# Performance work log

Measured on AMD Instinct MI355X. Metric: run time of the kernel, lower is better.

## Reference

```python
import jax, jax.numpy as jnp
import numpy as np

N = 50000   # nodes
F = 128     # v_feats
K = 128     # filters
H = 3       # multi_head
M = 10      # fixed neighbor count (hardcoded repeat(1,10,1) in source)


def setup_inputs() -> dict:
    key = jax.random.key(0)
    ks = jax.random.split(key, 10)
    vertices = jax.random.normal(ks[0], (N, F), jnp.float32)
    nh_indices = jax.random.randint(ks[1], (N, M), 0, N)
    int_indices = jax.random.randint(ks[2], (N, M), 0, N)
    nh_edges = jax.random.uniform(ks[3], (N, M), jnp.float32)
    int_edges = jax.random.uniform(ks[4], (N, M), jnp.float32)
    is_int = jax.random.randint(ks[5], (N,), 0, 2)
    scale = 0.05
    Wvc = jax.random.normal(ks[6], (H, F, K), jnp.float32) * scale
    Wvn_int = jax.random.normal(ks[7], (H, F, K), jnp.float32) * scale
    Wvn_nh = jax.random.normal(ks[8], (H, F, K), jnp.float32) * scale
    a = jax.random.normal(ks[9], (H, 2 * K, 1), jnp.float32) * scale
    bv = jnp.zeros((H, K), jnp.float32)
    return dict(vertices=vertices, nh_indices=nh_indices, int_indices=int_indices,
                nh_edges=nh_edges, int_edges=int_edges, is_int=is_int,
                Wvc=Wvc, bv=bv, Wvn_int=Wvn_int, Wvn_nh=Wvn_nh, a=a)


def reference(vertices, nh_indices, int_indices, nh_edges, int_edges, is_int,
              Wvc, bv, Wvn_int, Wvn_nh, a):
    n = vertices.shape[0]
    k = a.shape[1] // 2
    # Project center and neighbor features for all heads at once.
    Zc = jnp.einsum('nf,hfk->hnk', vertices, Wvc)        # [H,N,K]
    Vint = jnp.einsum('nf,hfk->hnk', vertices, Wvn_int)  # [H,N,K]
    Vnh = jnp.einsum('nf,hfk->hnk', vertices, Wvn_nh)    # [H,N,K]
    # cat((neighbor, center)) @ a  ==  neighbor @ a[:k] + center @ a[k:]
    a_n = a[:, :k, 0]  # [H,K]
    a_c = a[:, k:, 0]  # [H,K]
    e_center = jnp.einsum('hnk,hk->hn', Zc, a_c)[:, :, None]  # [H,N,1]

    def branch(Vside, idx, edges):
        mask = (idx != -1).astype(vertices.dtype)           # [N,M], -1 = pad
        g = Vside[:, idx]                                   # [H,N,M,K] gather
        e = jnp.einsum('hnmk,hk->hnm', g, a_n) + e_center   # [H,N,M]
        # faithful to source: scores zeroed (not -inf) by mask/edges before softmax
        e = e * mask[None] * edges[None]
        alpha = jax.nn.softmax(e, axis=2)                   # [H,N,M]
        norm = jnp.maximum(mask.sum(axis=1), 1.0)           # [N]
        Zn = jnp.einsum('hnmk,hnm->hnk', g * mask[None, :, :, None], alpha)
        return Zn / norm[None, :, None]

    Zn_inter = branch(Vint, int_indices, int_edges)
    Zn_chain = branch(Vnh, nh_indices, nh_edges)
    z = jax.nn.relu(Zc + Zn_inter + Zn_chain + bv[:, None, :])  # [H,N,K]
    # torch.cat(head outputs, dim=1) -> [N, H*K]
    return jnp.transpose(z, (1, 0, 2)).reshape(n, -1)
```

## Files before the change

### kernel.cpp

```cpp
#include <hip/hip_runtime.h>
#include <stdint.h>

#define N_V 50000
#define F_DIM 128
#define K_DIM 128
#define H_DIM 3
#define M_DIM 10
#define TILES_PER_BLK 4

using bf16x8 = __attribute__((ext_vector_type(8))) short;
using f32x4  = __attribute__((ext_vector_type(4))) float;
using f32x2  = __attribute__((ext_vector_type(2))) float;
using h4     = __attribute__((ext_vector_type(4))) _Float16;

__device__ inline unsigned short f2bf(float f) {
    union { float f; uint32_t u; } v; v.f = f;
    uint32_t u = v.u;
    u += 0x7fffu + ((u >> 16) & 1u);
    return (unsigned short)(u >> 16);
}

__device__ inline uint32_t pkh2(float a, float b) {
    union { _Float16 h[2]; uint32_t u; } v;
    v.h[0] = (_Float16)a; v.h[1] = (_Float16)b;
    return v.u;
}

#define LDS_AS __attribute__((address_space(3)))
__device__ inline void gl2lds16(const void* g, void* l) {
    __builtin_amdgcn_global_load_lds(
        (const __attribute__((address_space(1))) unsigned int*)g,
        (LDS_AS unsigned int*)l, 16, 0, 0);
}

#define WTOT (9 * 128 * 128)
#define XCH  (N_V * 16)
#define WACT (9 * 128)

__global__ void prep(const float* __restrict__ Wvc,
                     const float* __restrict__ Wvn_int,
                     const float* __restrict__ Wvn_nh,
                     const float* __restrict__ X,
                     const float* __restrict__ a,
                     unsigned short* __restrict__ Wt,
                     unsigned short* __restrict__ Xb,
                     unsigned short* __restrict__ wab) {
    int idx = blockIdx.x * 256 + threadIdx.x;
    if (idx < WTOT) {
        int b   = idx >> 14;
        int rem = idx & 16383;
        int k = rem >> 7;
        int f = rem & 127;
        int h = b / 3, t = b - 3 * h;
        const float* src = (t == 0) ? Wvc : (t == 1) ? Wvn_int : Wvn_nh;
        Wt[idx] = f2bf(src[(h * 128 + f) * 128 + k]);
        return;
    }
    int xi = idx - WTOT;
    if (xi < XCH) {
        const float4* Xv = (const float4*)X;
        float4 v0 = Xv[xi * 2];
        float4 v1 = Xv[xi * 2 + 1];
        uint4 o;
        o.x = (uint32_t)f2bf(v0.x) | ((uint32_t)f2bf(v0.y) << 16);
        o.y = (uint32_t)f2bf(v0.z) | ((uint32_t)f2bf(v0.w) << 16);
        o.z = (uint32_t)f2bf(v1.x) | ((uint32_t)f2bf(v1.y) << 16);
        o.w = (uint32_t)f2bf(v1.z) | ((uint32_t)f2bf(v1.w) << 16);
        *(uint4*)&Xb[(size_t)xi * 8] = o;
        return;
    }
    int wi = xi - XCH;
    if (wi < WACT) {
        int b = wi >> 7, f = wi & 127;
        int h = b / 3, t = b - 3 * h;
        const float* src = (t == 0) ? Wvc : (t == 1) ? Wvn_int : Wvn_nh;
        const float4* wrow = (const float4*)&src[(h * 128 + f) * 128];
        const float4* av   = (const float4*)&a[h * 256 + (t == 0 ? 128 : 0)];
        float acc = 0.f;
        #pragma unroll 8
        for (int c = 0; c < 32; ++c) {
            float4 w = wrow[c], x = av[c];
            acc += w.x * x.x + w.y * x.y + w.z * x.z + w.w * x.w;
        }
        wab[b * 128 + f] = f2bf(acc);
    }
}

__global__ __launch_bounds__(256, 3) void gemm_kernel(
    const unsigned short* __restrict__ Xb,
    const unsigned short* __restrict__ Wt,
    const unsigned short* __restrict__ wab,
    _Float16* __restrict__ zc16,
    uint8_t* __restrict__ Vint,
    uint8_t* __restrict__ Vnh,
    float* __restrict__ ec4,
    float* __restrict__ ei4,
    float* __restrict__ en4) {
    __shared__ unsigned short As[2][64 * 128];

    const int tid  = threadIdx.x;
    const int b    = blockIdx.y;
    const int hh   = b / 3;
    const int tt   = b - 3 * hh;
    const int wv   = tid >> 6;
    const int lane = tid & 63;
    const int q    = lane >> 4;
    const int ln   = lane & 15;
    const int cb   = (wv >> 1) * 64;
    const int rb   = (wv & 1) * 32;
    const int m0   = blockIdx.x * (64 * TILES_PER_BLK);

    auto stage = [&](int buf, int tile) {
        const int mb = m0 + tile * 64;
        #pragma unroll
        for (int it = 0; it < 4; ++it) {
            int c16 = it * 256 + tid;
            int r   = c16 >> 4;
            int p   = c16 & 15;
            int lch = p ^ (r & 15);
            int gr  = mb + r;
            if (gr >= N_V) gr = 0;
            gl2lds16(Xb + (size_t)gr * 128 + lch * 8, &As[buf][c16 * 8]);
        }
    };

    stage(0, 0);

    const unsigned short* Wb = Wt + (size_t)b * 16384;
    bf16x8 bfr[4][4];
    #pragma unroll
    for (int ct = 0; ct < 4; ++ct) {
        int col = cb + 4 * ln + ct;
        #pragma unroll
        for (int kk = 0; kk < 4; ++kk)
            bfr[ct][kk] = *(const bf16x8*)&Wb[col * 128 + kk * 32 + q * 8];
    }

    const bool do_e = (b == 0) && (wv < 2);
    bf16x8 wz[4];
    if (do_e) {
        #pragma unroll
        for (int kk = 0; kk < 4; ++kk) {
            bf16x8 z = {0, 0, 0, 0, 0, 0, 0, 0};
            if (ln < 9) z = *(const bf16x8*)&wab[ln * 128 + kk * 32 + q * 8];
            wz[kk] = z;
        }
    }

    __syncthreads();

    const int c0 = cb + 4 * ln;
    #pragma unroll
    for (int t = 0; t < TILES_PER_BLK; ++t) {
        const int mb = m0 + t * 64;

        if (t + 1 < TILES_PER_BLK) stage((t + 1) & 1, t + 1);

        bf16x8 afr[2][4];
        #pragma unroll
        for (int rt = 0; rt < 2; ++rt) {
            int r = rb + rt * 16 + ln;
            #pragma unroll
            for (int kk = 0; kk < 4; ++kk) {
                int p = (kk * 4 + q) ^ ln;
                afr[rt][kk] = *(const bf16x8*)&As[t & 1][r * 128 + p * 8];
            }
        }

        f32x4 acc[2][4];
        #pragma unroll
        for (int rt = 0; rt < 2; ++rt)
            #pragma unroll
            for (int ct = 0; ct < 4; ++ct) acc[rt][ct] = (f32x4){0.f, 0.f, 0.f, 0.f};

        #pragma unroll
        for (int rt = 0; rt < 2; ++rt)
            #pragma unroll
            for (int kk = 0; kk < 4; ++kk)
                #pragma unroll
                for (int ct = 0; ct < 4; ++ct)
                    acc[rt][ct] = __builtin_amdgcn_mfma_f32_16x16x32_bf16(
                        afr[rt][kk], bfr[ct][kk], acc[rt][ct], 0, 0, 0);

        if (do_e) {
            #pragma unroll
            for (int rt = 0; rt < 2; ++rt) {
                f32x4 ae = (f32x4){0.f, 0.f, 0.f, 0.f};
                #pragma unroll
                for (int kk = 0; kk < 4; ++kk)
                    ae = __builtin_amdgcn_mfma_f32_16x16x32_bf16(
                        afr[rt][kk], wz[kk], ae, 0, 0, 0);
                if (ln < 9) {
                    int h2 = ln / 3, t2 = ln - 3 * h2;
                    float* ep = (t2 == 0) ? ec4 : (t2 == 1) ? ei4 : en4;
                    #pragma unroll
                    for (int rg = 0; rg < 4; ++rg) {
                        int gr = mb + rb + rt * 16 + q * 4 + rg;
                        if (gr < N_V) ep[gr * 4 + h2] = ae[rg];
                    }
                }
            }
        }

        __syncthreads();

        if (tt == 0) {
            #pragma unroll
            for (int rt = 0; rt < 2; ++rt)
                #pragma unroll
                for (int rg = 0; rg < 4; ++rg) {
                    int gr = mb + rb + rt * 16 + q * 4 + rg;
                    if (gr >= N_V) continue;
                    uint2 s;
                    s.x = pkh2(acc[rt][0][rg], acc[rt][1][rg]);
                    s.y = pkh2(acc[rt][2][rg], acc[rt][3][rg]);
                    *(uint2*)&zc16[(size_t)gr * 384 + hh * 128 + c0] = s;
                }
        } else {
            uint8_t* Vside = (tt == 1) ? Vint : Vnh;
            #pragma unroll
            for (int rt = 0; rt < 2; ++rt)
                #pragma unroll
                for (int rg = 0; rg < 4; ++rg) {
                    int gr = mb + rb + rt * 16 + q * 4 + rg;
                    if (gr >= N_V) continue;
                    int pk = __builtin_amdgcn_cvt_pk_fp8_f32(
                        acc[rt][0][rg], acc[rt][1][rg], 0, false);
                    pk = __builtin_amdgcn_cvt_pk_fp8_f32(
                        acc[rt][2][rg], acc[rt][3][rg], pk, true);
                    *(uint32_t*)&Vside[((size_t)gr * 3 + hh) * 128 + c0] =
                        (uint32_t)pk;
                }
        }
    }
}

__global__ __launch_bounds__(256, 4) void attn_kernel(
    const int* __restrict__ nh_idx, const int* __restrict__ int_idx,
    const float* __restrict__ nh_edge, const float* __restrict__ int_edge,
    const float* __restrict__ bv,
    const uint8_t* __restrict__ Vint,
    const uint8_t* __restrict__ Vnh,
    const float* __restrict__ ec4, const float* __restrict__ ei4,
    const float* __restrict__ en4,
    const _Float16* __restrict__ zc16,
    float* __restrict__ out) {
    const int wv   = threadIdx.x >> 6;
    const int lane = threadIdx.x & 63;
    const int n    = blockIdx.x * 4 + wv;
    if (n >= N_V) return;
    const int g  = lane >> 4;
    const int gl = lane & 15;

    const bool part = (g <= 1) && (gl < M_DIM);
    int jm = -1; float wm = 0.f;
    if (part) {
        const int*   idx = (g == 0) ? int_idx  : nh_idx;
        const float* ed  = (g == 0) ? int_edge : nh_edge;
        jm = idx[n * M_DIM + gl];
        wm = ed[n * M_DIM + gl];
    }
    const bool  valid = part && (jm >= 0);
    const int   jc    = valid ? jm : 0;
    const float vfl   = valid ? 1.f : 0.f;

    const int src_base = (g < 2 ? 0 : 16) + (g & 1) * 5;
    int jrow[5];
    #pragma unroll
    for (int i = 0; i < 5; ++i) jrow[i] = __shfl(jc, src_base + i, 64);

    const uint8_t* Vb = (g < 2) ? Vint : Vnh;
    uint2 pv[3][5];
    #pragma unroll
    for (int i = 0; i < 5; ++i) {
        const uint8_t* base = Vb + (size_t)jrow[i] * 384 + gl * 8;
        #pragma unroll
        for (int h = 0; h < H_DIM; ++h)
            pv[h][i] = *(const uint2*)(base + h * 128);
    }
    float4 ev = make_float4(0.f, 0.f, 0.f, 0.f);
    if (part) ev = *(const float4*)&(((g == 0) ? ei4 : en4)[jc * 4]);
    const float4 ecv = *(const float4*)&ec4[n * 4];

    float4 zc[3], bb[3];
    if (g < 2) {
        #pragma unroll
        for (int h = 0; h < H_DIM; ++h) {
            h4 z = *(const h4*)&zc16[(size_t)n * 384 + h * 128 + gl * 8 + g * 4];
            zc[h] = make_float4((float)z[0], (float)z[1], (float)z[2], (float)z[3]);
            bb[h] = *(const float4*)&bv[h * 128 + gl * 8 + g * 4];
        }
    }

    float cf = vfl;
    #pragma unroll
    for (int off = 1; off < 16; off <<= 1) cf += __shfl_xor(cf, off, 64);
    const float cnorm = fmaxf(cf, 1.f);

    __builtin_amdgcn_sched_barrier(0);

    #pragma unroll
    for (int h = 0; h < H_DIM; ++h) {
        const float eh  = (h == 0) ? ev.x  : (h == 1) ? ev.y  : ev.z;
        const float ech = (h == 0) ? ecv.x : (h == 1) ? ecv.y : ecv.z;

        float l = (part && valid) ? (eh + ech) * wm : 0.f;
        float ex = part ? __expf(l) : 0.f;
        float sv = ex;
        #pragma unroll
        for (int off = 1; off < 16; off <<= 1) sv += __shfl_xor(sv, off, 64);
        float alphap = valid ? ex / (sv * cnorm) : 0.f;

        f32x2 acc2[4];
        #pragma unroll
        for (int c = 0; c < 4; ++c) acc2[c] = (f32x2){0.f, 0.f};
        #pragma unroll
        for (int i = 0; i < 5; ++i) {
            float al = __shfl(alphap, src_base + i, 64);
            f32x2 al2 = (f32x2){al, al};
            uint2 p  = pv[h][i];
            f32x2 f01 = __builtin_amdgcn_cvt_pk_f32_fp8(p.x, false);
            f32x2 f23 = __builtin_amdgcn_cvt_pk_f32_fp8(p.x, true);
            f32x2 f45 = __builtin_amdgcn_cvt_pk_f32_fp8(p.y, false);
            f32x2 f67 = __builtin_amdgcn_cvt_pk_f32_fp8(p.y, true);
            acc2[0] += al2 * f01;
            acc2[1] += al2 * f23;
            acc2[2] += al2 * f45;
            acc2[3] += al2 * f67;
        }
        #pragma unroll
        for (int c = 0; c < 4; ++c) {
            f32x2 v = acc2[c];
            v.x += __shfl_xor(v.x, 16, 64);
            v.y += __shfl_xor(v.y, 16, 64);
            v.x += __shfl_xor(v.x, 32, 64);
            v.y += __shfl_xor(v.y, 32, 64);
            acc2[c] = v;
        }
        if (g < 2) {
            size_t o = (size_t)n * 384 + h * 128 + gl * 8 + g * 4;
            float4 zn;
            if (g == 0) zn = make_float4(acc2[0].x, acc2[0].y, acc2[1].x, acc2[1].y);
            else        zn = make_float4(acc2[2].x, acc2[2].y, acc2[3].x, acc2[3].y);
            float4 r;
            r.x = fmaxf(zc[h].x + zn.x + bb[h].x, 0.f);
            r.y = fmaxf(zc[h].y + zn.y + bb[h].y, 0.f);
            r.z = fmaxf(zc[h].z + zn.z + bb[h].z, 0.f);
            r.w = fmaxf(zc[h].w + zn.w + bb[h].w, 0.f);
            *(float4*)&out[o] = r;
        }
    }
}

extern "C" void kernel_launch(void* const* d_in, const int* in_sizes, int n_in,
                              void* d_out, int out_size, void* d_ws, size_t ws_size,
                              hipStream_t stream) {
    const float* vertices    = (const float*)d_in[0];
    const int*   nh_indices  = (const int*)d_in[1];
    const int*   int_indices = (const int*)d_in[2];
    const float* nh_edges    = (const float*)d_in[3];
    const float* int_edges   = (const float*)d_in[4];
    const float* Wvc     = (const float*)d_in[6];
    const float* bv      = (const float*)d_in[7];
    const float* Wvn_int = (const float*)d_in[8];
    const float* Wvn_nh  = (const float*)d_in[9];
    const float* a       = (const float*)d_in[10];
    float* out = (float*)d_out;

    char* ws = (char*)d_ws;
    size_t off = 0;
    unsigned short* Wt = (unsigned short*)(ws + off);
    off += (size_t)WTOT * 2;                  off = (off + 255) & ~(size_t)255;
    unsigned short* wab = (unsigned short*)(ws + off);
    off += (size_t)WACT * 2;                  off = (off + 255) & ~(size_t)255;
    unsigned short* Xb = (unsigned short*)(ws + off);
    off += (size_t)N_V * 128 * 2;             off = (off + 255) & ~(size_t)255;
    uint8_t* Vint = (uint8_t*)(ws + off);
    off += (size_t)H_DIM * N_V * 128;         off = (off + 255) & ~(size_t)255;
    uint8_t* Vnh = (uint8_t*)(ws + off);
    off += (size_t)H_DIM * N_V * 128;         off = (off + 255) & ~(size_t)255;
    _Float16* zc16 = (_Float16*)(ws + off);
    off += (size_t)N_V * 384 * 2;             off = (off + 255) & ~(size_t)255;
    float* ec4 = (float*)(ws + off);
    off += (size_t)N_V * 4 * 4;               off = (off + 255) & ~(size_t)255;
    float* ei4 = (float*)(ws + off);
    off += (size_t)N_V * 4 * 4;               off = (off + 255) & ~(size_t)255;
    float* en4 = (float*)(ws + off);
    off += (size_t)N_V * 4 * 4;

    int prep_threads = WTOT + XCH + WACT;
    prep<<<(prep_threads + 255) / 256, 256, 0, stream>>>(
        Wvc, Wvn_int, Wvn_nh, vertices, a, Wt, Xb, wab);

    dim3 grid_g((N_V + 64 * TILES_PER_BLK - 1) / (64 * TILES_PER_BLK), 9);
    gemm_kernel<<<grid_g, 256, 0, stream>>>(Xb, Wt, wab, zc16, Vint, Vnh,
                                            ec4, ei4, en4);

    attn_kernel<<<(N_V + 3) / 4, 256, 0, stream>>>(
        nh_indices, int_indices, nh_edges, int_edges, bv,
        Vint, Vnh, ec4, ei4, en4, zc16, out);
}
```

Baseline: 230.7 us.

## Fuse bf16 conversion and attention-score projection into GEMM, drop prep kernel

Removes the separate prep kernel. The GEMM now reads fp32 vertices and weights directly and converts them to bf16 in registers before staging into LDS. The attention-score dot products are now computed from the GEMM accumulators times the coefficient vector, using shuffle reductions and LDS atomics, instead of a separate MFMA pass against precomputed W·a vectors. The grid is remapped to a 1D index with blocks grouped per XCD so that blocks sharing an X tile land on the same XCD for L2 reuse. The costs are synchronous global loads in place of async global-to-LDS copies, strided uncoalesced weight loads per block, and duplicated conversion work across the 9 head/type blocks.

Result: no change. 234.6 us (+1.7%).

```diff
diff --git a/kernel.cpp b/kernel.cpp
--- a/kernel.cpp
+++ b/kernel.cpp
@@ -1,4 +1,5 @@
 #include <hip/hip_runtime.h>
+#include <hip/hip_bf16.h>
 #include <stdint.h>
 
 #define N_V 50000
@@ -7,89 +8,33 @@
 #define H_DIM 3
 #define M_DIM 10
 #define TILES_PER_BLK 4
+#define NBLK 1764
+#define BLK_PER_XCD 221
+#define NBLK_PAD 1768
 
 using bf16x8 = __attribute__((ext_vector_type(8))) short;
 using f32x4  = __attribute__((ext_vector_type(4))) float;
 using f32x2  = __attribute__((ext_vector_type(2))) float;
 using h4     = __attribute__((ext_vector_type(4))) _Float16;
 
-__device__ inline unsigned short f2bf(float f) {
-    union { float f; uint32_t u; } v; v.f = f;
-    uint32_t u = v.u;
-    u += 0x7fffu + ((u >> 16) & 1u);
-    return (unsigned short)(u >> 16);
-}
-
 __device__ inline uint32_t pkh2(float a, float b) {
     union { _Float16 h[2]; uint32_t u; } v;
     v.h[0] = (_Float16)a; v.h[1] = (_Float16)b;
     return v.u;
 }
 
-#define LDS_AS __attribute__((address_space(3)))
-__device__ inline void gl2lds16(const void* g, void* l) {
-    __builtin_amdgcn_global_load_lds(
-        (const __attribute__((address_space(1))) unsigned int*)g,
-        (LDS_AS unsigned int*)l, 16, 0, 0);
-}
-
-#define WTOT (9 * 128 * 128)
-#define XCH  (N_V * 16)
-#define WACT (9 * 128)
-
-__global__ void prep(const float* __restrict__ Wvc,
-                     const float* __restrict__ Wvn_int,
-                     const float* __restrict__ Wvn_nh,
-                     const float* __restrict__ X,
-                     const float* __restrict__ a,
-                     unsigned short* __restrict__ Wt,
-                     unsigned short* __restrict__ Xb,
-                     unsigned short* __restrict__ wab) {
-    int idx = blockIdx.x * 256 + threadIdx.x;
-    if (idx < WTOT) {
-        int b   = idx >> 14;
-        int rem = idx & 16383;
-        int k = rem >> 7;
-        int f = rem & 127;
-        int h = b / 3, t = b - 3 * h;
-        const float* src = (t == 0) ? Wvc : (t == 1) ? Wvn_int : Wvn_nh;
-        Wt[idx] = f2bf(src[(h * 128 + f) * 128 + k]);
-        return;
-    }
-    int xi = idx - WTOT;
-    if (xi < XCH) {
-        const float4* Xv = (const float4*)X;
-        float4 v0 = Xv[xi * 2];
-        float4 v1 = Xv[xi * 2 + 1];
-        uint4 o;
-        o.x = (uint32_t)f2bf(v0.x) | ((uint32_t)f2bf(v0.y) << 16);
-        o.y = (uint32_t)f2bf(v0.z) | ((uint32_t)f2bf(v0.w) << 16);
-        o.z = (uint32_t)f2bf(v1.x) | ((uint32_t)f2bf(v1.y) << 16);
-        o.w = (uint32_t)f2bf(v1.z) | ((uint32_t)f2bf(v1.w) << 16);
-        *(uint4*)&Xb[(size_t)xi * 8] = o;
-        return;
-    }
-    int wi = xi - XCH;
-    if (wi < WACT) {
-        int b = wi >> 7, f = wi & 127;
-        int h = b / 3, t = b - 3 * h;
-        const float* src = (t == 0) ? Wvc : (t == 1) ? Wvn_int : Wvn_nh;
-        const float4* wrow = (const float4*)&src[(h * 128 + f) * 128];
-        const float4* av   = (const float4*)&a[h * 256 + (t == 0 ? 128 : 0)];
-        float acc = 0.f;
-        #pragma unroll 8
-        for (int c = 0; c < 32; ++c) {
-            float4 w = wrow[c], x = av[c];
-            acc += w.x * x.x + w.y * x.y + w.z * x.z + w.w * x.w;
-        }
-        wab[b * 128 + f] = f2bf(acc);
-    }
+__device__ inline uint32_t pkbf2(float a, float b) {
+    __hip_bfloat162 p = __float22bfloat162_rn(make_float2(a, b));
+    union { __hip_bfloat162 h; uint32_t u; } v; v.h = p;
+    return v.u;
 }
 
 __global__ __launch_bounds__(256, 3) void gemm_kernel(
-    const unsigned short* __restrict__ Xb,
-    const unsigned short* __restrict__ Wt,
-    const unsigned short* __restrict__ wab,
+    const float* __restrict__ X,
+    const float* __restrict__ Wvc,
+    const float* __restrict__ Wvn_int,
+    const float* __restrict__ Wvn_nh,
+    const float* __restrict__ a,
     _Float16* __restrict__ zc16,
     uint8_t* __restrict__ Vint,
     uint8_t* __restrict__ Vnh,
@@ -97,54 +42,84 @@
     float* __restrict__ ei4,
     float* __restrict__ en4) {
     __shared__ unsigned short As[2][64 * 128];
+    __shared__ float e_part[TILES_PER_BLK][64];
+
+    const int c = blockIdx.x & 7;
+    const int s = blockIdx.x >> 3;
+    const int g = c * BLK_PER_XCD + s;
+    if (g >= NBLK) return;
+    const int x  = g / 9;
+    const int b  = g - 9 * x;
+    const int hh = b / 3;
+    const int tt = b - 3 * hh;
 
     const int tid  = threadIdx.x;
-    const int b    = blockIdx.y;
-    const int hh   = b / 3;
-    const int tt   = b - 3 * hh;
     const int wv   = tid >> 6;
     const int lane = tid & 63;
     const int q    = lane >> 4;
     const int ln   = lane & 15;
     const int cb   = (wv >> 1) * 64;
     const int rb   = (wv & 1) * 32;
-    const int m0   = blockIdx.x * (64 * TILES_PER_BLK);
+    const int m0   = x * (64 * TILES_PER_BLK);
+
+    const float* Wb = ((tt == 0) ? Wvc : (tt == 1) ? Wvn_int : Wvn_nh)
+                      + (size_t)hh * 16384;
 
     auto stage = [&](int buf, int tile) {
         const int mb = m0 + tile * 64;
+        float4 xa[4], xb[4];
+        int lc[4];
         #pragma unroll
         for (int it = 0; it < 4; ++it) {
-            int c16 = it * 256 + tid;
-            int r   = c16 >> 4;
-            int p   = c16 & 15;
-            int lch = p ^ (r & 15);
-            int gr  = mb + r;
+            int ch = it * 256 + tid;
+            int r  = ch >> 4;
+            int pg = ch & 15;
+            int gr = mb + r;
             if (gr >= N_V) gr = 0;
-            gl2lds16(Xb + (size_t)gr * 128 + lch * 8, &As[buf][c16 * 8]);
+            const float4* src = (const float4*)(X + (size_t)gr * 128 + pg * 8);
+            xa[it] = src[0];
+            xb[it] = src[1];
+            lc[it] = (r * 16 + (pg ^ (r & 15))) * 8;
+        }
+        #pragma unroll
+        for (int it = 0; it < 4; ++it) {
+            uint4 o;
+            o.x = pkbf2(xa[it].x, xa[it].y);
+            o.y = pkbf2(xa[it].z, xa[it].w);
+            o.z = pkbf2(xb[it].x, xb[it].y);
+            o.w = pkbf2(xb[it].z, xb[it].w);
+            *(uint4*)&As[buf][lc[it]] = o;
         }
     };
 
     stage(0, 0);
 
-    const unsigned short* Wb = Wt + (size_t)b * 16384;
     bf16x8 bfr[4][4];
     #pragma unroll
     for (int ct = 0; ct < 4; ++ct) {
-        int col = cb + 4 * ln + ct;
-        #pragma unroll
-        for (int kk = 0; kk < 4; ++kk)
-            bfr[ct][kk] = *(const bf16x8*)&Wb[col * 128 + kk * 32 + q * 8];
-    }
-
-    const bool do_e = (b == 0) && (wv < 2);
-    bf16x8 wz[4];
-    if (do_e) {
+        const int col = cb + 4 * ln + ct;
         #pragma unroll
         for (int kk = 0; kk < 4; ++kk) {
-            bf16x8 z = {0, 0, 0, 0, 0, 0, 0, 0};
-            if (ln < 9) z = *(const bf16x8*)&wab[ln * 128 + kk * 32 + q * 8];
-            wz[kk] = z;
-        }
+            const float* wp = Wb + (size_t)(kk * 32 + q * 8) * 128 + col;
+            float v0 = wp[0 * 128], v1 = wp[1 * 128], v2 = wp[2 * 128], v3 = wp[3 * 128];
+            float v4 = wp[4 * 128], v5 = wp[5 * 128], v6 = wp[6 * 128], v7 = wp[7 * 128];
+            union { uint32_t u[4]; bf16x8 v; } pk;
+            pk.u[0] = pkbf2(v0, v1);
+            pk.u[1] = pkbf2(v2, v3);
+            pk.u[2] = pkbf2(v4, v5);
+            pk.u[3] = pkbf2(v6, v7);
+            bfr[ct][kk] = pk.v;
+        }
+    }
+
+    const float* av = a + hh * 256 + (tt == 0 ? 128 : 0);
+    float acoef[4];
+    #pragma unroll
+    for (int ct = 0; ct < 4; ++ct) acoef[ct] = av[cb + 4 * ln + ct];
+
+    if (tid < 64) {
+        #pragma unroll
+        for (int t = 0; t < TILES_PER_BLK; ++t) e_part[t][tid] = 0.f;
     }
 
     __syncthreads();
@@ -156,49 +131,40 @@
 
         if (t + 1 < TILES_PER_BLK) stage((t + 1) & 1, t + 1);
 
-        bf16x8 afr[2][4];
+        f32x4 acc[2][4];
+        #pragma unroll
+        for (int rt = 0; rt < 2; ++rt)
+            #pragma unroll
+            for (int ct = 0; ct < 4; ++ct) acc[rt][ct] = (f32x4){0.f, 0.f, 0.f, 0.f};
+
         #pragma unroll
         for (int rt = 0; rt < 2; ++rt) {
-            int r = rb + rt * 16 + ln;
+            bf16x8 afr[4];
+            const int r = rb + rt * 16 + ln;
             #pragma unroll
             for (int kk = 0; kk < 4; ++kk) {
                 int p = (kk * 4 + q) ^ ln;
-                afr[rt][kk] = *(const bf16x8*)&As[t & 1][r * 128 + p * 8];
+                afr[kk] = *(const bf16x8*)&As[t & 1][r * 128 + p * 8];
             }
-        }
-
-        f32x4 acc[2][4];
-        #pragma unroll
-        for (int rt = 0; rt < 2; ++rt)
-            #pragma unroll
-            for (int ct = 0; ct < 4; ++ct) acc[rt][ct] = (f32x4){0.f, 0.f, 0.f, 0.f};
-
-        #pragma unroll
-        for (int rt = 0; rt < 2; ++rt)
             #pragma unroll
             for (int kk = 0; kk < 4; ++kk)
                 #pragma unroll
                 for (int ct = 0; ct < 4; ++ct)
                     acc[rt][ct] = __builtin_amdgcn_mfma_f32_16x16x32_bf16(
-                        afr[rt][kk], bfr[ct][kk], acc[rt][ct], 0, 0, 0);
-
-        if (do_e) {
-            #pragma unroll
-            for (int rt = 0; rt < 2; ++rt) {
-                f32x4 ae = (f32x4){0.f, 0.f, 0.f, 0.f};
+                        afr[kk], bfr[ct][kk], acc[rt][ct], 0, 0, 0);
+        }
+
+        #pragma unroll
+        for (int rt = 0; rt < 2; ++rt) {
+            #pragma unroll
+            for (int rg = 0; rg < 4; ++rg) {
+                float p = acc[rt][0][rg] * acoef[0] + acc[rt][1][rg] * acoef[1]
+                        + acc[rt][2][rg] * acoef[2] + acc[rt][3][rg] * acoef[3];
                 #pragma unroll
-                for (int kk = 0; kk < 4; ++kk)
-                    ae = __builtin_amdgcn_mfma_f32_16x16x32_bf16(
-                        afr[rt][kk], wz[kk], ae, 0, 0, 0);
-                if (ln < 9) {
-                    int h2 = ln / 3, t2 = ln - 3 * h2;
-                    float* ep = (t2 == 0) ? ec4 : (t2 == 1) ? ei4 : en4;
-                    #pragma unroll
-                    for (int rg = 0; rg < 4; ++rg) {
-                        int gr = mb + rb + rt * 16 + q * 4 + rg;
-                        if (gr < N_V) ep[gr * 4 + h2] = ae[rg];
-                    }
-                }
+                for (int off = 1; off < 16; off <<= 1)
+                    p += __shfl_xor(p, off, 64);
+                if (ln == 0)
+                    atomicAdd(&e_part[t][rb + rt * 16 + q * 4 + rg], p);
             }
         }
 
@@ -211,10 +177,10 @@
                 for (int rg = 0; rg < 4; ++rg) {
                     int gr = mb + rb + rt * 16 + q * 4 + rg;
                     if (gr >= N_V) continue;
-                    uint2 s;
-                    s.x = pkh2(acc[rt][0][rg], acc[rt][1][rg]);
-                    s.y = pkh2(acc[rt][2][rg], acc[rt][3][rg]);
-                    *(uint2*)&zc16[(size_t)gr * 384 + hh * 128 + c0] = s;
+                    uint2 sv;
+                    sv.x = pkh2(acc[rt][0][rg], acc[rt][1][rg]);
+                    sv.y = pkh2(acc[rt][2][rg], acc[rt][3][rg]);
+                    *(uint2*)&zc16[(size_t)gr * 384 + hh * 128 + c0] = sv;
                 }
         } else {
             uint8_t* Vside = (tt == 1) ? Vint : Vnh;
@@ -233,9 +199,18 @@
                 }
         }
     }
-}
-
-__global__ __launch_bounds__(256, 4) void attn_kernel(
+
+    {
+        int ti = tid >> 6, r = tid & 63;
+        int gr = m0 + ti * 64 + r;
+        if (gr < N_V) {
+            float* ep = (tt == 0) ? ec4 : (tt == 1) ? ei4 : en4;
+            ep[gr * 4 + hh] = e_part[ti][r];
+        }
+    }
+}
+
+__global__ __launch_bounds__(256) void attn_kernel(
     const int* __restrict__ nh_idx, const int* __restrict__ int_idx,
     const float* __restrict__ nh_edge, const float* __restrict__ int_edge,
     const float* __restrict__ bv,
@@ -297,8 +272,6 @@
     for (int off = 1; off < 16; off <<= 1) cf += __shfl_xor(cf, off, 64);
     const float cnorm = fmaxf(cf, 1.f);
 
-    __builtin_amdgcn_sched_barrier(0);
-
     #pragma unroll
     for (int h = 0; h < H_DIM; ++h) {
         const float eh  = (h == 0) ? ev.x  : (h == 1) ? ev.y  : ev.z;
@@ -369,12 +342,6 @@
 
     char* ws = (char*)d_ws;
     size_t off = 0;
-    unsigned short* Wt = (unsigned short*)(ws + off);
-    off += (size_t)WTOT * 2;                  off = (off + 255) & ~(size_t)255;
-    unsigned short* wab = (unsigned short*)(ws + off);
-    off += (size_t)WACT * 2;                  off = (off + 255) & ~(size_t)255;
-    unsigned short* Xb = (unsigned short*)(ws + off);
-    off += (size_t)N_V * 128 * 2;             off = (off + 255) & ~(size_t)255;
     uint8_t* Vint = (uint8_t*)(ws + off);
     off += (size_t)H_DIM * N_V * 128;         off = (off + 255) & ~(size_t)255;
     uint8_t* Vnh = (uint8_t*)(ws + off);
@@ -388,13 +355,9 @@
     float* en4 = (float*)(ws + off);
     off += (size_t)N_V * 4 * 4;
 
-    int prep_threads = WTOT + XCH + WACT;
-    prep<<<(prep_threads + 255) / 256, 256, 0, stream>>>(
-        Wvc, Wvn_int, Wvn_nh, vertices, a, Wt, Xb, wab);
-
-    dim3 grid_g((N_V + 64 * TILES_PER_BLK - 1) / (64 * TILES_PER_BLK), 9);
-    gemm_kernel<<<grid_g, 256, 0, stream>>>(Xb, Wt, wab, zc16, Vint, Vnh,
-                                            ec4, ei4, en4);
+    gemm_kernel<<<NBLK_PAD, 256, 0, stream>>>(
+        vertices, Wvc, Wvn_int, Wvn_nh, a,
+        zc16, Vint, Vnh, ec4, ei4, en4);
 
     attn_kernel<<<(N_V + 3) / 4, 256, 0, stream>>>(
         nh_indices, int_indices, nh_edges, int_edges, bv,
```
